# Kernel optimization log

Hardware: AMD Instinct MI355X
Metric: run time of the kernel (lower is better)

The kernel has to match this reference:

```python
import jax, jax.numpy as jnp
import numpy as np

NUM_HEADS = 16
HEAD_DIM = 64
HIDDEN = NUM_HEADS * HEAD_DIM


def setup_inputs() -> dict:
    key = jax.random.key(0)
    ks = jax.random.split(key, 10)
    B, S = 4, 4096
    return {
        "x": jax.random.normal(ks[0], (B, S, HIDDEN), dtype=jnp.float32),
        "Wq": jax.random.normal(ks[1], (HIDDEN, HIDDEN), dtype=jnp.float32) * 0.02,
        "bq": jax.random.normal(ks[2], (HIDDEN,), dtype=jnp.float32) * 0.02,
        "Wk": jax.random.normal(ks[3], (HIDDEN, HIDDEN), dtype=jnp.float32) * 0.02,
        "bk": jax.random.normal(ks[4], (HIDDEN,), dtype=jnp.float32) * 0.02,
        "Wv": jax.random.normal(ks[5], (HIDDEN, HIDDEN), dtype=jnp.float32) * 0.02,
        "bv": jax.random.normal(ks[6], (HIDDEN,), dtype=jnp.float32) * 0.02,
        "Wo": jax.random.normal(ks[7], (HIDDEN, HIDDEN), dtype=jnp.float32) * 0.02,
        "bo": jax.random.normal(ks[8], (HIDDEN,), dtype=jnp.float32) * 0.02,
        "scale": jax.random.normal(ks[9], (HEAD_DIM,), dtype=jnp.float32),
    }


def reference(x, Wq, bq, Wk, bk, Wv, bv, Wo, bo, scale):
    B, S, _ = x.shape
    # Linear layers (torch Linear: y = x @ W.T + b)
    q = (x @ Wq.T + bq).reshape(B, S, NUM_HEADS, HEAD_DIM)
    k = (x @ Wk.T + bk).reshape(B, S, NUM_HEADS, HEAD_DIM)
    v = (x @ Wv.T + bv).reshape(B, S, NUM_HEADS, HEAD_DIM)
    q = q * scale  # per-head-dim learned scale
    # NOTE: original torch code never moves heads to dim 1, so matmul
    # contracts over head_dim, giving per-token head-to-head scores [B,S,H,H].
    inv_sqrt_d = 1.0 / np.sqrt(HEAD_DIM).astype(np.float32)
    scores = jnp.einsum('bshd,bstd->bsht', q, k) * inv_sqrt_d  # [B,S,H,H]
    attn = jax.nn.softmax(scores, axis=-1)
    out = jnp.einsum('bsht,bstd->bshd', attn, v).reshape(B, S, HIDDEN)
    return out @ Wo.T + bo
```

## Files before the change

kernel.cpp:

```cpp
#include <hip/hip_runtime.h>
#include <hip/hip_fp16.h>
#include <cstdint>
#include <cstddef>

#define NHEAD 16
#define HDIM  64
#define HID   1024

using f16x8 = __attribute__((ext_vector_type(8))) _Float16;
using f32x4 = __attribute__((ext_vector_type(4))) float;

typedef const __attribute__((address_space(1))) unsigned int* gq_t;
typedef __attribute__((address_space(3))) unsigned int* lq_t;

__global__ void cvt_f32_f16(const float* __restrict__ in, _Float16* __restrict__ out, int n8) {
    for (int i = blockIdx.x * blockDim.x + threadIdx.x; i < n8; i += gridDim.x * blockDim.x) {
        const float4* p = (const float4*)(in + (size_t)i * 8);
        float4 a = p[0], b = p[1];
        f16x8 o;
        o[0] = (_Float16)a.x; o[1] = (_Float16)a.y; o[2] = (_Float16)a.z; o[3] = (_Float16)a.w;
        o[4] = (_Float16)b.x; o[5] = (_Float16)b.y; o[6] = (_Float16)b.z; o[7] = (_Float16)b.w;
        *(f16x8*)(out + (size_t)i * 8) = o;
    }
}

template <typename OutT>
__global__ __launch_bounds__(256, 2)
void gemm_bt(const _Float16* __restrict__ A, const _Float16* __restrict__ Bw,
             const float* __restrict__ bias, OutT* __restrict__ C,
             int M, int N, int K)
{
    __shared__ _Float16 As[128 * 64];
    __shared__ _Float16 Bs[128 * 64];

    const int tid  = threadIdx.x;
    const int lane = tid & 63;
    const int wid  = tid >> 6;
    const int wm   = wid >> 1;
    const int wn   = wid & 1;
    const int m0   = blockIdx.y * 128;
    const int n0   = blockIdx.x * 128;

    f32x4 acc[4][4] = {};

    const int r_in  = lane >> 3;
    const int s_lds = lane & 7;

    for (int k0 = 0; k0 < K; k0 += 64) {
        #pragma unroll
        for (int j = 0; j < 4; ++j) {
            const int rbase = j * 32 + wid * 8;
            const int r     = rbase + r_in;
            const int s_g   = s_lds ^ (r & 7);
            const _Float16* ga = A  + (size_t)(m0 + r) * K + k0 + s_g * 8;
            const _Float16* gb = Bw + (size_t)(n0 + r) * K + k0 + s_g * 8;
            __builtin_amdgcn_global_load_lds((gq_t)(const void*)ga,
                                             (lq_t)(void*)(As + rbase * 64), 16, 0, 0);
            __builtin_amdgcn_global_load_lds((gq_t)(const void*)gb,
                                             (lq_t)(void*)(Bs + rbase * 64), 16, 0, 0);
        }
        __syncthreads();

        const int g = lane >> 4;
        #pragma unroll
        for (int kk = 0; kk < 2; ++kk) {
            f16x8 af[4], bf[4];
            #pragma unroll
            for (int mi = 0; mi < 4; ++mi) {
                const int row  = wm * 64 + mi * 16 + (lane & 15);
                const int slot = (kk * 4 + g) ^ (row & 7);
                af[mi] = *(const f16x8*)&As[row * 64 + slot * 8];
            }
            #pragma unroll
            for (int ni = 0; ni < 4; ++ni) {
                const int row  = wn * 64 + ni * 16 + (lane & 15);
                const int slot = (kk * 4 + g) ^ (row & 7);
                bf[ni] = *(const f16x8*)&Bs[row * 64 + slot * 8];
            }
            #pragma unroll
            for (int mi = 0; mi < 4; ++mi)
                #pragma unroll
                for (int ni = 0; ni < 4; ++ni)
                    acc[mi][ni] = __builtin_amdgcn_mfma_f32_16x16x32_f16(
                        af[mi], bf[ni], acc[mi][ni], 0, 0, 0);
        }
        __syncthreads();
    }

    #pragma unroll
    for (int ni = 0; ni < 4; ++ni) {
        const int col = n0 + wn * 64 + ni * 16 + (lane & 15);
        const float bv = bias[col];
        #pragma unroll
        for (int mi = 0; mi < 4; ++mi) {
            const int rowb = m0 + wm * 64 + mi * 16 + (lane >> 4) * 4;
            #pragma unroll
            for (int q = 0; q < 4; ++q) {
                const float val = acc[mi][ni][q] + bv;
                C[(size_t)(rowb + q) * N + col] = (OutT)val;
            }
        }
    }
}

__global__ __launch_bounds__(128, 2)
void attn_kernel(const _Float16* __restrict__ qkv, const float* __restrict__ scale,
                 _Float16* __restrict__ out)
{
    __shared__ _Float16 kv[8][2048];
    __shared__ float sc[64];

    const int tid  = threadIdx.x;
    const int tok0 = blockIdx.x * 8;

    if (tid < 64) sc[tid] = scale[tid];

    #pragma unroll
    for (int it = 0; it < 16; ++it) {
        const int vid = tid + it * 128;
        const int tok = vid >> 8;
        const int ofs = (vid & 255) * 8;
        *(f16x8*)&kv[tok][ofs] =
            *(const f16x8*)&qkv[(size_t)(tok0 + tok) * 3072 + 1024 + ofs];
    }
    __syncthreads();

    const int tok = tid >> 4;
    const int h   = tid & 15;
    const size_t qbase = (size_t)(tok0 + tok) * 3072 + h * 64;

    float q[64];
    #pragma unroll
    for (int d0 = 0; d0 < 64; d0 += 8) {
        f16x8 qv = *(const f16x8*)&qkv[qbase + d0];
        #pragma unroll
        for (int j = 0; j < 8; ++j) q[d0 + j] = (float)qv[j] * sc[d0 + j];
    }

    float s[16];
    #pragma unroll
    for (int t = 0; t < 16; ++t) {
        float a = 0.f;
        #pragma unroll
        for (int d0 = 0; d0 < 64; d0 += 8) {
            f16x8 kvv = *(const f16x8*)&kv[tok][t * 64 + d0];
            #pragma unroll
            for (int j = 0; j < 8; ++j) a += q[d0 + j] * (float)kvv[j];
        }
        s[t] = a * 0.125f;
    }

    float mx = s[0];
    #pragma unroll
    for (int t = 1; t < 16; ++t) mx = fmaxf(mx, s[t]);
    float sum = 0.f;
    #pragma unroll
    for (int t = 0; t < 16; ++t) { s[t] = __expf(s[t] - mx); sum += s[t]; }
    const float inv = 1.f / sum;

    float o[64] = {};
    #pragma unroll
    for (int t = 0; t < 16; ++t) {
        const float a = s[t] * inv;
        #pragma unroll
        for (int d0 = 0; d0 < 64; d0 += 8) {
            f16x8 vv = *(const f16x8*)&kv[tok][1024 + t * 64 + d0];
            #pragma unroll
            for (int j = 0; j < 8; ++j) o[d0 + j] += a * (float)vv[j];
        }
    }

    #pragma unroll
    for (int d0 = 0; d0 < 64; d0 += 8) {
        f16x8 ov;
        #pragma unroll
        for (int j = 0; j < 8; ++j) ov[j] = (_Float16)o[d0 + j];
        *(f16x8*)&out[(size_t)(tok0 + tok) * 1024 + h * 64 + d0] = ov;
    }
}

extern "C" void kernel_launch(void* const* d_in, const int* in_sizes, int n_in,
                              void* d_out, int out_size, void* d_ws, size_t ws_size,
                              hipStream_t stream)
{
    const float* x     = (const float*)d_in[0];
    const float* Wq    = (const float*)d_in[1];
    const float* bq    = (const float*)d_in[2];
    const float* Wk    = (const float*)d_in[3];
    const float* bk    = (const float*)d_in[4];
    const float* Wv    = (const float*)d_in[5];
    const float* bv    = (const float*)d_in[6];
    const float* Wo    = (const float*)d_in[7];
    const float* bo    = (const float*)d_in[8];
    const float* scale = (const float*)d_in[9];
    float* out = (float*)d_out;

    const int M = in_sizes[0] / HID;

    char* ws = (char*)d_ws;
    _Float16* x16    = (_Float16*)ws;
    _Float16* attn16 = x16;
    _Float16* wqkv16 = (_Float16*)(ws + (size_t)M * HID * 2);
    _Float16* wo16   = wqkv16 + (size_t)3 * HID * HID;
    float*    bqkv   = (float*)(wo16 + (size_t)HID * HID);
    _Float16* qkv16  = (_Float16*)((char*)bqkv + 3 * HID * 4);

    hipMemcpyAsync(bqkv,            bq, HID * 4, hipMemcpyDeviceToDevice, stream);
    hipMemcpyAsync(bqkv + HID,      bk, HID * 4, hipMemcpyDeviceToDevice, stream);
    hipMemcpyAsync(bqkv + 2 * HID,  bv, HID * 4, hipMemcpyDeviceToDevice, stream);

    cvt_f32_f16<<<4096, 256, 0, stream>>>(x,  x16,                 M * HID / 8);
    cvt_f32_f16<<<1024, 256, 0, stream>>>(Wq, wqkv16,              HID * HID / 8);
    cvt_f32_f16<<<1024, 256, 0, stream>>>(Wk, wqkv16 + HID * HID,  HID * HID / 8);
    cvt_f32_f16<<<1024, 256, 0, stream>>>(Wv, wqkv16 + 2*HID*HID,  HID * HID / 8);
    cvt_f32_f16<<<1024, 256, 0, stream>>>(Wo, wo16,                HID * HID / 8);

    gemm_bt<_Float16><<<dim3(3 * HID / 128, M / 128), 256, 0, stream>>>(
        x16, wqkv16, bqkv, qkv16, M, 3 * HID, HID);

    attn_kernel<<<M / 8, 128, 0, stream>>>(qkv16, scale, attn16);

    gemm_bt<float><<<dim3(HID / 128, M / 128), 256, 0, stream>>>(
        attn16, wo16, bo, out, M, HID, HID);
}
```

Before: 233.7 us.

## Replace GEMM with 256x256-tile 8-wave double-buffered pipelined kernel

Replaces the 128x128 single-buffered GEMM with a 256x256 tile kernel using 8 waves, a 128KB double-buffered LDS, and an interleaved schedule. In that schedule global-to-LDS loads for the next K-steps are issued between quarter-tile MFMA blocks, with explicit vmcnt/lgkmcnt waits, barriers and setprio. The goal is to hide global load latency behind MFMA work and raise data reuse per tile. The cost is fewer blocks: the QKV GEMM gets 12x64 tiles and the output GEMM 4x64 tiles, only 256 blocks, which may underfill 256 CUs. The hand-scheduled waits also carry correctness risk.

New measurement: 235.9 us. About the same (+1.0%).

```diff
diff --git a/kernel.cpp b/kernel.cpp
--- a/kernel.cpp
+++ b/kernel.cpp
@@ -24,79 +24,133 @@
     }
 }
 
+
+#define VMCNT4  asm volatile("s_waitcnt vmcnt(4)" ::: "memory")
+#define VMCNT0  asm volatile("s_waitcnt vmcnt(0)" ::: "memory")
+#define LGKM0   asm volatile("s_waitcnt lgkmcnt(0)" ::: "memory")
+#define BAR     __builtin_amdgcn_s_barrier()
+
+#define READ_A(MH) { \
+    const int base = buf * 32768 + (MH) * 8192 + (wm * 64) * 64; \
+    _Pragma("unroll") for (int mi = 0; mi < 4; ++mi) { \
+        const int rl = mi * 16 + l15; \
+        _Pragma("unroll") for (int kk = 0; kk < 2; ++kk) { \
+            const int slot = (kk * 4 + g) ^ l7; \
+            a[mi][kk] = *(const f16x8*)&lds[base + rl * 64 + slot * 8]; \
+        } } }
+
+#define READ_B(NH, BREG) { \
+    const int base = buf * 32768 + 16384 + (NH) * 8192 + (wn * 32) * 64; \
+    _Pragma("unroll") for (int ni = 0; ni < 2; ++ni) { \
+        const int rl = ni * 16 + l15; \
+        _Pragma("unroll") for (int kk = 0; kk < 2; ++kk) { \
+            const int slot = (kk * 4 + g) ^ l7; \
+            BREG[ni][kk] = *(const f16x8*)&lds[base + rl * 64 + slot * 8]; \
+        } } }
+
+#define STAGE_A(T, MH) if ((T) < NT) { \
+    const int bufS = (T) & 1; \
+    _Pragma("unroll") for (int s = 0; s < 2; ++s) { \
+        const int rho = s * 64 + wid * 8 + r_in; \
+        const int r = ((rho >> 6) << 7) + (MH) * 64 + (rho & 63); \
+        const int sg = s_l ^ r_in; \
+        const _Float16* src = A + (size_t)(m0 + r) * K + (size_t)(T) * 64 + sg * 8; \
+        _Float16* dst = (_Float16*)&lds[bufS * 32768 + (MH) * 8192 + (s * 64 + wid * 8) * 64]; \
+        __builtin_amdgcn_global_load_lds((gq_t)(const void*)src, (lq_t)(void*)dst, 16, 0, 0); \
+    } }
+
+#define STAGE_B(T, NH) if ((T) < NT) { \
+    const int bufS = (T) & 1; \
+    _Pragma("unroll") for (int s = 0; s < 2; ++s) { \
+        const int rho = s * 64 + wid * 8 + r_in; \
+        const int r = ((rho >> 5) << 6) + (NH) * 32 + (rho & 31); \
+        const int sg = s_l ^ r_in; \
+        const _Float16* src = Bw + (size_t)(n0 + r) * K + (size_t)(T) * 64 + sg * 8; \
+        _Float16* dst = (_Float16*)&lds[bufS * 32768 + 16384 + (NH) * 8192 + (s * 64 + wid * 8) * 64]; \
+        __builtin_amdgcn_global_load_lds((gq_t)(const void*)src, (lq_t)(void*)dst, 16, 0, 0); \
+    } }
+
+#define MFMA_QUAD(MO, NO, BREG) \
+    __builtin_amdgcn_s_setprio(1); \
+    _Pragma("unroll") for (int mi = 0; mi < 4; ++mi) \
+    _Pragma("unroll") for (int ni = 0; ni < 2; ++ni) \
+    _Pragma("unroll") for (int kk = 0; kk < 2; ++kk) \
+        acc[(MO) + mi][(NO) + ni] = __builtin_amdgcn_mfma_f32_16x16x32_f16( \
+            a[mi][kk], BREG[ni][kk], acc[(MO) + mi][(NO) + ni], 0, 0, 0); \
+    __builtin_amdgcn_s_setprio(0);
+
 template <typename OutT>
-__global__ __launch_bounds__(256, 2)
-void gemm_bt(const _Float16* __restrict__ A, const _Float16* __restrict__ Bw,
-             const float* __restrict__ bias, OutT* __restrict__ C,
-             int M, int N, int K)
+__global__ __launch_bounds__(512, 2)
+void gemm_bt8(const _Float16* __restrict__ A, const _Float16* __restrict__ Bw,
+              const float* __restrict__ bias, OutT* __restrict__ C,
+              int M, int N, int K)
 {
-    __shared__ _Float16 As[128 * 64];
-    __shared__ _Float16 Bs[128 * 64];
+    __shared__ _Float16 lds[65536];
 
     const int tid  = threadIdx.x;
     const int lane = tid & 63;
     const int wid  = tid >> 6;
-    const int wm   = wid >> 1;
-    const int wn   = wid & 1;
-    const int m0   = blockIdx.y * 128;
-    const int n0   = blockIdx.x * 128;
-
-    f32x4 acc[4][4] = {};
-
-    const int r_in  = lane >> 3;
-    const int s_lds = lane & 7;
-
-    for (int k0 = 0; k0 < K; k0 += 64) {
-        #pragma unroll
-        for (int j = 0; j < 4; ++j) {
-            const int rbase = j * 32 + wid * 8;
-            const int r     = rbase + r_in;
-            const int s_g   = s_lds ^ (r & 7);
-            const _Float16* ga = A  + (size_t)(m0 + r) * K + k0 + s_g * 8;
-            const _Float16* gb = Bw + (size_t)(n0 + r) * K + k0 + s_g * 8;
-            __builtin_amdgcn_global_load_lds((gq_t)(const void*)ga,
-                                             (lq_t)(void*)(As + rbase * 64), 16, 0, 0);
-            __builtin_amdgcn_global_load_lds((gq_t)(const void*)gb,
-                                             (lq_t)(void*)(Bs + rbase * 64), 16, 0, 0);
-        }
-        __syncthreads();
-
-        const int g = lane >> 4;
-        #pragma unroll
-        for (int kk = 0; kk < 2; ++kk) {
-            f16x8 af[4], bf[4];
-            #pragma unroll
-            for (int mi = 0; mi < 4; ++mi) {
-                const int row  = wm * 64 + mi * 16 + (lane & 15);
-                const int slot = (kk * 4 + g) ^ (row & 7);
-                af[mi] = *(const f16x8*)&As[row * 64 + slot * 8];
-            }
-            #pragma unroll
-            for (int ni = 0; ni < 4; ++ni) {
-                const int row  = wn * 64 + ni * 16 + (lane & 15);
-                const int slot = (kk * 4 + g) ^ (row & 7);
-                bf[ni] = *(const f16x8*)&Bs[row * 64 + slot * 8];
-            }
-            #pragma unroll
-            for (int mi = 0; mi < 4; ++mi)
-                #pragma unroll
-                for (int ni = 0; ni < 4; ++ni)
-                    acc[mi][ni] = __builtin_amdgcn_mfma_f32_16x16x32_f16(
-                        af[mi], bf[ni], acc[mi][ni], 0, 0, 0);
-        }
-        __syncthreads();
-    }
-
-    #pragma unroll
-    for (int ni = 0; ni < 4; ++ni) {
-        const int col = n0 + wn * 64 + ni * 16 + (lane & 15);
+    const int wm   = wid >> 2;
+    const int wn   = wid & 3;
+    const int m0   = blockIdx.y * 256;
+    const int n0   = blockIdx.x * 256;
+    const int NT   = K >> 6;
+
+    const int l15  = lane & 15;
+    const int l7   = lane & 7;
+    const int g    = lane >> 4;
+    const int r_in = lane >> 3;
+    const int s_l  = lane & 7;
+
+    f32x4 acc[8][4] = {};
+    f16x8 a[4][2], b0[2][2], b1[2][2];
+
+    STAGE_A(0, 0); STAGE_B(0, 0); STAGE_B(0, 1); STAGE_A(0, 1);
+    STAGE_A(1, 0); STAGE_B(1, 0);
+    VMCNT4;
+    BAR;
+
+    for (int t = 0; t < NT; ++t) {
+        const int buf = t & 1;
+
+        READ_A(0); READ_B(0, b0);
+        STAGE_B(t + 1, 1);
+        BAR;
+        LGKM0; __builtin_amdgcn_sched_barrier(0);
+        MFMA_QUAD(0, 0, b0);
+        BAR;
+
+        READ_B(1, b1);
+        STAGE_A(t + 1, 1);
+        BAR;
+        LGKM0; __builtin_amdgcn_sched_barrier(0);
+        MFMA_QUAD(0, 2, b1);
+        BAR;
+
+        READ_A(1);
+        STAGE_A(t + 2, 0);
+        BAR;
+        LGKM0; __builtin_amdgcn_sched_barrier(0);
+        MFMA_QUAD(4, 0, b0);
+        BAR;
+
+        STAGE_B(t + 2, 0);
+        if (t == NT - 2) { VMCNT0; } else { VMCNT4; }
+        BAR;
+        MFMA_QUAD(4, 2, b1);
+        BAR;
+    }
+
+    #pragma unroll
+    for (int an = 0; an < 4; ++an) {
+        const int col = n0 + wn * 64 + (an >> 1) * 32 + (an & 1) * 16 + l15;
         const float bv = bias[col];
         #pragma unroll
-        for (int mi = 0; mi < 4; ++mi) {
-            const int rowb = m0 + wm * 64 + mi * 16 + (lane >> 4) * 4;
+        for (int am = 0; am < 8; ++am) {
+            const int rowb = m0 + wm * 128 + (am >> 2) * 64 + (am & 3) * 16 + (lane >> 4) * 4;
             #pragma unroll
             for (int q = 0; q < 4; ++q) {
-                const float val = acc[mi][ni][q] + bv;
+                const float val = acc[am][an][q] + bv;
                 C[(size_t)(rowb + q) * N + col] = (OutT)val;
             }
         }
@@ -205,21 +259,21 @@
     float*    bqkv   = (float*)(wo16 + (size_t)HID * HID);
     _Float16* qkv16  = (_Float16*)((char*)bqkv + 3 * HID * 4);
 
-    hipMemcpyAsync(bqkv,            bq, HID * 4, hipMemcpyDeviceToDevice, stream);
-    hipMemcpyAsync(bqkv + HID,      bk, HID * 4, hipMemcpyDeviceToDevice, stream);
-    hipMemcpyAsync(bqkv + 2 * HID,  bv, HID * 4, hipMemcpyDeviceToDevice, stream);
-
-    cvt_f32_f16<<<4096, 256, 0, stream>>>(x,  x16,                 M * HID / 8);
-    cvt_f32_f16<<<1024, 256, 0, stream>>>(Wq, wqkv16,              HID * HID / 8);
-    cvt_f32_f16<<<1024, 256, 0, stream>>>(Wk, wqkv16 + HID * HID,  HID * HID / 8);
-    cvt_f32_f16<<<1024, 256, 0, stream>>>(Wv, wqkv16 + 2*HID*HID,  HID * HID / 8);
-    cvt_f32_f16<<<1024, 256, 0, stream>>>(Wo, wo16,                HID * HID / 8);
-
-    gemm_bt<_Float16><<<dim3(3 * HID / 128, M / 128), 256, 0, stream>>>(
+    hipMemcpyAsync(bqkv,           bq, HID * 4, hipMemcpyDeviceToDevice, stream);
+    hipMemcpyAsync(bqkv + HID,     bk, HID * 4, hipMemcpyDeviceToDevice, stream);
+    hipMemcpyAsync(bqkv + 2 * HID, bv, HID * 4, hipMemcpyDeviceToDevice, stream);
+
+    cvt_f32_f16<<<4096, 256, 0, stream>>>(x,  x16,                M * HID / 8);
+    cvt_f32_f16<<<1024, 256, 0, stream>>>(Wq, wqkv16,             HID * HID / 8);
+    cvt_f32_f16<<<1024, 256, 0, stream>>>(Wk, wqkv16 + HID * HID, HID * HID / 8);
+    cvt_f32_f16<<<1024, 256, 0, stream>>>(Wv, wqkv16 + 2*HID*HID, HID * HID / 8);
+    cvt_f32_f16<<<1024, 256, 0, stream>>>(Wo, wo16,               HID * HID / 8);
+
+    gemm_bt8<_Float16><<<dim3(3 * HID / 256, M / 256), 512, 0, stream>>>(
         x16, wqkv16, bqkv, qkv16, M, 3 * HID, HID);
 
     attn_kernel<<<M / 8, 128, 0, stream>>>(qkv16, scale, attn16);
 
-    gemm_bt<float><<<dim3(HID / 128, M / 128), 256, 0, stream>>>(
+    gemm_bt8<float><<<dim3(HID / 256, M / 256), 512, 0, stream>>>(
         attn16, wo16, bo, out, M, HID, HID);
 }
```
